# Optimization experiments

Measured on AMD Instinct MI355X. Metric: run time of the kernel, lower is better.

Reference implementation:

```python
import jax, jax.numpy as jnp
import numpy as np

N, E, F, H, C = 50000, 800000, 602, 32, 41
BN_EPS = 1e-5


def _mlp(h, Wa, ba, Wb, bb):
    return jax.nn.relu(h @ Wa + ba) @ Wb + bb


def _bn(h, gamma, beta):
    # BatchNorm1d training mode: per-feature batch mean / biased variance
    m = jnp.mean(h, axis=0)
    v = jnp.var(h, axis=0)
    return (h - m) * jax.lax.rsqrt(v + BN_EPS) * gamma + beta


def _gin(x, row, col, Wa, ba, Wb, bb):
    # sum-aggregate neighbor features (SpMM via gather + segment_sum), eps=0
    agg = jax.ops.segment_sum(x[col], row, num_segments=x.shape[0])
    return _mlp(x + agg, Wa, ba, Wb, bb)


def setup_inputs() -> dict:
    key = jax.random.key(0)
    ks = jax.random.split(key, 16)
    s = 0.05
    inp = {
        "x": jax.random.normal(ks[0], (N, F), dtype=jnp.float32),
        "row": jax.random.randint(ks[1], (E,), 0, N),
        "col": jax.random.randint(ks[2], (E,), 0, N),
        # conv1 MLP
        "W1a": jax.random.normal(ks[3], (F, H), dtype=jnp.float32) * s,
        "b1a": jnp.zeros((H,), jnp.float32),
        "W1b": jax.random.normal(ks[4], (H, H), dtype=jnp.float32) * s,
        "b1b": jnp.zeros((H,), jnp.float32),
        "g1": jnp.ones((H,), jnp.float32),
        "be1": jnp.zeros((H,), jnp.float32),
        # conv2 MLP
        "W2a": jax.random.normal(ks[5], (H, H), dtype=jnp.float32) * s,
        "b2a": jnp.zeros((H,), jnp.float32),
        "W2b": jax.random.normal(ks[6], (H, H), dtype=jnp.float32) * s,
        "b2b": jnp.zeros((H,), jnp.float32),
        "g2": jnp.ones((H,), jnp.float32),
        "be2": jnp.zeros((H,), jnp.float32),
        # heads
        "Wf1": jax.random.normal(ks[7], (H, H), dtype=jnp.float32) * s,
        "bf1": jnp.zeros((H,), jnp.float32),
        "Wf2": jax.random.normal(ks[8], (H, C), dtype=jnp.float32) * s,
        "bf2": jnp.zeros((C,), jnp.float32),
    }
    return inp


def reference(x, row, col, W1a, b1a, W1b, b1b, g1, be1,
              W2a, b2a, W2b, b2b, g2, be2, Wf1, bf1, Wf2, bf2):
    h = _bn(_gin(x, row, col, W1a, b1a, W1b, b1b), g1, be1)
    h = _bn(_gin(h, row, col, W2a, b2a, W2b, b2b), g2, be2)
    h = jax.nn.relu(h @ Wf1 + bf1)
    return h @ Wf2 + bf2
```

## Files before the change

### kernel.cpp

```cpp
#include <hip/hip_runtime.h>
#include <hip/hip_bf16.h>

#define N_NODES 50000
#define F_IN    602
#define H_DIM   32
#define C_OUT   41
#define E_EDGES 800000
#define BN_EPS  1e-5f

__global__ __launch_bounds__(256) void k_gemm_in_v3(
    const float* __restrict__ x, const float* __restrict__ W,
    float* __restrict__ p) {
  __shared__ float xs[64 * 68];
  __shared__ float ws[32 * 68];
  const int tid = threadIdx.x;
  const int r0 = blockIdx.x * 64;

  const int cg  = tid & 15;
  const int rgg = tid >> 4;

  const int srow = tid >> 5;
  const int fe   = tid & 31;

  const float* xrp[8];
  #pragma unroll
  for (int pp = 0; pp < 8; pp++) {
    int rr = r0 + pp * 8 + srow;
    if (rr > N_NODES - 1) rr = N_NODES - 1;
    xrp[pp] = x + (size_t)rr * F_IN;
  }

  float2 xr[8];
  float4 wr[2];

  #pragma unroll
  for (int pp = 0; pp < 8; pp++)
    xr[pp] = *(const float2*)(xrp[pp] + 2 * fe);
  #pragma unroll
  for (int q = 0; q < 2; q++)
    wr[q] = *(const float4*)(W + q * 1024 + 4 * tid);

  float acc[4][2] = {};

  for (int ch = 0; ch < 10; ch++) {
    __syncthreads();
    #pragma unroll
    for (int pp = 0; pp < 8; pp++)
      *(float2*)&xs[(pp * 8 + srow) * 68 + 2 * fe] = xr[pp];
    #pragma unroll
    for (int q = 0; q < 2; q++) {
      int off = q * 1024 + 4 * tid;
      int kk = off >> 5, c0 = off & 31;
      ws[(c0 + 0) * 68 + kk] = wr[q].x;
      ws[(c0 + 1) * 68 + kk] = wr[q].y;
      ws[(c0 + 2) * 68 + kk] = wr[q].z;
      ws[(c0 + 3) * 68 + kk] = wr[q].w;
    }
    __syncthreads();
    if (ch < 9) {
      const int k0 = (ch + 1) * 64;
      #pragma unroll
      for (int pp = 0; pp < 8; pp++) {
        int k = k0 + 2 * fe;
        float2 v = {0.f, 0.f};
        if (k + 2 <= F_IN) v = *(const float2*)(xrp[pp] + k);
        xr[pp] = v;
      }
      #pragma unroll
      for (int q = 0; q < 2; q++) {
        int off = k0 * H_DIM + q * 1024 + 4 * tid;
        float4 v = {0.f, 0.f, 0.f, 0.f};
        if (off < F_IN * H_DIM) v = *(const float4*)(W + off);
        wr[q] = v;
      }
    }
    #pragma unroll
    for (int kq = 0; kq < 16; kq++) {
      float4 xv[4], wv[2];
      #pragma unroll
      for (int i = 0; i < 4; i++) xv[i] = *(float4*)&xs[(rgg + 16 * i) * 68 + kq * 4];
      #pragma unroll
      for (int j = 0; j < 2; j++) wv[j] = *(float4*)&ws[(cg + 16 * j) * 68 + kq * 4];
      #pragma unroll
      for (int i = 0; i < 4; i++)
        #pragma unroll
        for (int j = 0; j < 2; j++)
          acc[i][j] += xv[i].x * wv[j].x + xv[i].y * wv[j].y +
                       xv[i].z * wv[j].z + xv[i].w * wv[j].w;
    }
  }

  #pragma unroll
  for (int i = 0; i < 4; i++) {
    int gr = r0 + rgg + 16 * i;
    if (gr < N_NODES) {
      #pragma unroll
      for (int j = 0; j < 2; j++)
        p[(size_t)gr * H_DIM + cg + 16 * j] = acc[i][j];
    }
  }
}

__global__ __launch_bounds__(256) void k_hist(const int* __restrict__ row,
                                              int* __restrict__ deg) {
  int e = blockIdx.x * 256 + threadIdx.x;
  if (e < E_EDGES) atomicAdd(&deg[row[e]], 1);
}

__global__ __launch_bounds__(256) void k_scanA(const int* __restrict__ deg,
                                               int* __restrict__ start,
                                               int* __restrict__ bsum) {
  __shared__ int sc[256];
  int t = threadIdx.x, i = blockIdx.x * 256 + t;
  int v = (i < N_NODES) ? deg[i] : 0;
  sc[t] = v;
  __syncthreads();
  #pragma unroll
  for (int off = 1; off < 256; off <<= 1) {
    int u = (t >= off) ? sc[t - off] : 0;
    __syncthreads();
    sc[t] += u;
    __syncthreads();
  }
  if (i < N_NODES) start[i] = sc[t] - v;
  if (t == 255) bsum[blockIdx.x] = sc[255];
}

__global__ __launch_bounds__(256) void k_scanB(const int* __restrict__ bsum,
                                               int* __restrict__ boff, int nb) {
  __shared__ int sc[256];
  int t = threadIdx.x;
  int v = (t < nb) ? bsum[t] : 0;
  sc[t] = v;
  __syncthreads();
  #pragma unroll
  for (int off = 1; off < 256; off <<= 1) {
    int u = (t >= off) ? sc[t - off] : 0;
    __syncthreads();
    sc[t] += u;
    __syncthreads();
  }
  if (t < nb) boff[t] = sc[t] - v;
}

__global__ __launch_bounds__(256) void k_scanC(int* __restrict__ start,
                                               const int* __restrict__ boff,
                                               int* __restrict__ cursor) {
  int i = blockIdx.x * 256 + threadIdx.x;
  if (i < N_NODES) {
    int s = start[i] + boff[blockIdx.x];
    start[i] = s;
    cursor[i] = s;
  }
  if (i == 0) start[N_NODES] = E_EDGES;
}

__global__ __launch_bounds__(256) void k_fill(const int* __restrict__ row,
                                              const int* __restrict__ col,
                                              int* __restrict__ cursor,
                                              int* __restrict__ ecol) {
  int e = blockIdx.x * 256 + threadIdx.x;
  if (e < E_EDGES) {
    int pos = atomicAdd(&cursor[row[e]], 1);
    ecol[pos] = col[e];
  }
}

__global__ __launch_bounds__(256) void k_gather(
    const float* __restrict__ p, const float* __restrict__ b,
    const int* __restrict__ start, const int* __restrict__ ecol,
    float* __restrict__ z) {
  int hw = (blockIdx.x * 256 + threadIdx.x) >> 5;
  int c = threadIdx.x & 31;
  if (hw >= N_NODES) return;
  int s = start[hw], e = start[hw + 1];
  float acc = p[(size_t)hw * H_DIM + c] + b[c];
  int i = s;
  for (; i + 3 < e; i += 4) {
    int s0 = ecol[i], s1 = ecol[i + 1], s2 = ecol[i + 2], s3 = ecol[i + 3];
    float v0 = p[(size_t)s0 * H_DIM + c];
    float v1 = p[(size_t)s1 * H_DIM + c];
    float v2 = p[(size_t)s2 * H_DIM + c];
    float v3 = p[(size_t)s3 * H_DIM + c];
    acc += v0; acc += v1; acc += v2; acc += v3;
  }
  for (; i < e; i++) acc += p[(size_t)ecol[i] * H_DIM + c];
  z[(size_t)hw * H_DIM + c] = acc;
}

__global__ __launch_bounds__(256) void k_zinit(const float* __restrict__ p,
                                               const float* __restrict__ b,
                                               float* __restrict__ z) {
  int i = blockIdx.x * 256 + threadIdx.x;
  if (i < N_NODES * H_DIM) z[i] = p[i] + b[i & 31];
}

__global__ __launch_bounds__(256) void k_scatter(
    const int* __restrict__ row, const int* __restrict__ col,
    const float* __restrict__ p, float* __restrict__ z) {
  long long t = (long long)blockIdx.x * 256 + threadIdx.x;
  int e = (int)(t >> 5);
  int c = (int)(t & 31);
  if (e < E_EDGES) {
    int s = col[e], d = row[e];
    atomicAdd(&z[(size_t)d * H_DIM + c], p[(size_t)s * H_DIM + c]);
  }
}

__global__ __launch_bounds__(256) void k_mlp_stats(
    const float* __restrict__ z, const float* __restrict__ W,
    const float* __restrict__ b, float* __restrict__ hpre,
    float* __restrict__ stats) {
  __shared__ float as_[64 * 36];
  __shared__ float ws[32 * 36];
  __shared__ float red[512];
  const int tid = threadIdx.x;
  for (int i = tid; i < 1024; i += 256) {
    int k = i >> 5, c = i & 31;
    ws[c * 36 + k] = W[(size_t)k * H_DIM + c];
  }
  const int r0 = blockIdx.x * 64;
  for (int i = tid; i < 2048; i += 256) {
    int r = i >> 5, c = i & 31;
    int gr = r0 + r;
    float v = (gr < N_NODES) ? z[(size_t)gr * H_DIM + c] : 0.f;
    as_[r * 36 + c] = fmaxf(v, 0.f);
  }
  __syncthreads();
  const int c = tid & 31, rg = tid >> 5;
  float4 wc[8];
  #pragma unroll
  for (int q = 0; q < 8; q++) wc[q] = *(float4*)&ws[c * 36 + q * 4];
  const float bc = b[c];
  float lsum = 0.f, lsq = 0.f;
  #pragma unroll
  for (int i = 0; i < 8; i++) {
    int r = rg * 8 + i;
    float a = bc;
    #pragma unroll
    for (int q = 0; q < 8; q++) {
      float4 h4 = *(float4*)&as_[r * 36 + q * 4];
      a += h4.x * wc[q].x + h4.y * wc[q].y + h4.z * wc[q].z + h4.w * wc[q].w;
    }
    int gr = r0 + r;
    if (gr < N_NODES) {
      hpre[(size_t)gr * H_DIM + c] = a;
      lsum += a; lsq += a * a;
    }
  }
  __syncthreads();
  red[tid] = lsum; red[256 + tid] = lsq;
  __syncthreads();
  if (tid < 32) {
    float s = 0.f, q = 0.f;
    #pragma unroll
    for (int g = 0; g < 8; g++) { s += red[g * 32 + tid]; q += red[256 + g * 32 + tid]; }
    atomicAdd(&stats[tid], s);
    atomicAdd(&stats[32 + tid], q);
  }
}

__global__ __launch_bounds__(256) void k_gemm32_affine(
    const float* __restrict__ hpre, const float* __restrict__ stats,
    const float* __restrict__ g, const float* __restrict__ be,
    const float* __restrict__ W, float* __restrict__ p) {
  __shared__ float hs[64 * 36];
  __shared__ float ws[32 * 36];
  __shared__ float ssl[64];
  const int tid = threadIdx.x;
  if (tid < 32) {
    float m = stats[tid] * (1.f / N_NODES);
    float v = stats[32 + tid] * (1.f / N_NODES) - m * m;
    float sc = g[tid] * rsqrtf(v + BN_EPS);
    ssl[tid] = sc;
    ssl[32 + tid] = be[tid] - m * sc;
  }
  for (int i = tid; i < 1024; i += 256) {
    int k = i >> 5, c = i & 31;
    ws[c * 36 + k] = W[(size_t)k * H_DIM + c];
  }
  __syncthreads();
  const int r0 = blockIdx.x * 64;
  for (int i = tid; i < 2048; i += 256) {
    int r = i >> 5, c = i & 31;
    int gr = r0 + r;
    float v = (gr < N_NODES) ? hpre[(size_t)gr * H_DIM + c] * ssl[c] + ssl[32 + c] : 0.f;
    hs[r * 36 + c] = v;
  }
  __syncthreads();
  const int c = tid & 31, rg = tid >> 5;
  float4 wc[8];
  #pragma unroll
  for (int q = 0; q < 8; q++) wc[q] = *(float4*)&ws[c * 36 + q * 4];
  #pragma unroll
  for (int i = 0; i < 8; i++) {
    int r = rg * 8 + i;
    float a = 0.f;
    #pragma unroll
    for (int q = 0; q < 8; q++) {
      float4 h4 = *(float4*)&hs[r * 36 + q * 4];
      a += h4.x * wc[q].x + h4.y * wc[q].y + h4.z * wc[q].z + h4.w * wc[q].w;
    }
    int gr = r0 + r;
    if (gr < N_NODES) p[(size_t)gr * H_DIM + c] = a;
  }
}

__global__ __launch_bounds__(256) void k_heads(
    const float* __restrict__ hpre, const float* __restrict__ stats,
    const float* __restrict__ g, const float* __restrict__ be,
    const float* __restrict__ W1, const float* __restrict__ b1,
    const float* __restrict__ W2, const float* __restrict__ b2,
    float* __restrict__ out) {
  __shared__ float hs[64 * 36];
  __shared__ float fs[64 * 36];
  __shared__ float w1[32 * 36];
  __shared__ float w2[41 * 36];
  __shared__ float ssl[64];
  const int tid = threadIdx.x;
  if (tid < 32) {
    float m = stats[tid] * (1.f / N_NODES);
    float v = stats[32 + tid] * (1.f / N_NODES) - m * m;
    float sc = g[tid] * rsqrtf(v + BN_EPS);
    ssl[tid] = sc;
    ssl[32 + tid] = be[tid] - m * sc;
  }
  for (int i = tid; i < 1024; i += 256) {
    int k = i >> 5, c = i & 31;
    w1[c * 36 + k] = W1[(size_t)k * H_DIM + c];
  }
  for (int i = tid; i < 41 * 32; i += 256) {
    int j = i >> 5, k = i & 31;
    w2[j * 36 + k] = W2[(size_t)k * C_OUT + j];
  }
  __syncthreads();
  const int r0 = blockIdx.x * 64;
  for (int i = tid; i < 2048; i += 256) {
    int r = i >> 5, c = i & 31;
    int gr = r0 + r;
    hs[r * 36 + c] = (gr < N_NODES) ? hpre[(size_t)gr * H_DIM + c] * ssl[c] + ssl[32 + c] : 0.f;
  }
  __syncthreads();
  {
    const int c = tid & 31, rg = tid >> 5;
    float4 wc[8];
    #pragma unroll
    for (int q = 0; q < 8; q++) wc[q] = *(float4*)&w1[c * 36 + q * 4];
    const float bc = b1[c];
    #pragma unroll
    for (int i = 0; i < 8; i++) {
      int r = rg * 8 + i;
      float a = bc;
      #pragma unroll
      for (int q = 0; q < 8; q++) {
        float4 h4 = *(float4*)&hs[r * 36 + q * 4];
        a += h4.x * wc[q].x + h4.y * wc[q].y + h4.z * wc[q].z + h4.w * wc[q].w;
      }
      fs[r * 36 + c] = fmaxf(a, 0.f);
    }
  }
  __syncthreads();
  for (int idx = tid; idx < 64 * C_OUT; idx += 256) {
    int r = idx / C_OUT, j = idx - r * C_OUT;
    int gr = r0 + r;
    if (gr < N_NODES) {
      float a = b2[j];
      #pragma unroll
      for (int q = 0; q < 8; q++) {
        float4 f4 = *(float4*)&fs[r * 36 + q * 4];
        float4 w4 = *(float4*)&w2[j * 36 + q * 4];
        a += f4.x * w4.x + f4.y * w4.y + f4.z * w4.z + f4.w * w4.w;
      }
      out[(size_t)gr * C_OUT + j] = a;
    }
  }
}

extern "C" void kernel_launch(void* const* d_in, const int* in_sizes, int n_in,
                              void* d_out, int out_size, void* d_ws, size_t ws_size,
                              hipStream_t stream) {
  const float* x   = (const float*)d_in[0];
  const int* row   = (const int*)d_in[1];
  const int* col   = (const int*)d_in[2];
  const float* W1a = (const float*)d_in[3];
  const float* b1a = (const float*)d_in[4];
  const float* W1b = (const float*)d_in[5];
  const float* b1b = (const float*)d_in[6];
  const float* g1  = (const float*)d_in[7];
  const float* be1 = (const float*)d_in[8];
  const float* W2a = (const float*)d_in[9];
  const float* b2a = (const float*)d_in[10];
  const float* W2b = (const float*)d_in[11];
  const float* b2b = (const float*)d_in[12];
  const float* g2  = (const float*)d_in[13];
  const float* be2 = (const float*)d_in[14];
  const float* Wf1 = (const float*)d_in[15];
  const float* bf1 = (const float*)d_in[16];
  const float* Wf2 = (const float*)d_in[17];
  const float* bf2 = (const float*)d_in[18];
  float* out = (float*)d_out;

  float* ws = (float*)d_ws;
  const size_t NH = (size_t)N_NODES * H_DIM;
  float* pA    = ws;
  float* zB    = ws + NH;
  float* hC    = ws + 2 * NH;
  float* stats = ws + 3 * NH;
  int*   startA = (int*)(ws + 3 * NH + 256);
  int*   cursor = startA + 50016;
  int*   deg    = cursor + 50016;
  int*   ecol   = deg + 50016;
  int*   bsum   = ecol + E_EDGES;
  int*   boff   = bsum + 256;
  const size_t need_bytes = ((3 * NH + 256) + 3 * 50016 + E_EDGES + 512) * 4;
  const bool use_csr = (ws_size >= need_bytes);

  hipMemsetAsync(stats, 0, 128 * sizeof(float), stream);

  const int g64   = (N_NODES + 63) / 64;
  const int gE    = (E_EDGES + 255) / 256;
  const int gN    = (N_NODES + 255) / 256;
  const int gHW   = (N_NODES * 32 + 255) / 256;
  const int gScat = (E_EDGES * 32 + 255) / 256;

  if (use_csr) {
    hipMemsetAsync(deg, 0, 50000 * sizeof(int), stream);
    k_hist <<<gE, 256, 0, stream>>>(row, deg);
    k_scanA<<<gN, 256, 0, stream>>>(deg, startA, bsum);
    k_scanB<<<1, 256, 0, stream>>>(bsum, boff, gN);
    k_scanC<<<gN, 256, 0, stream>>>(startA, boff, cursor);
    k_fill <<<gE, 256, 0, stream>>>(row, col, cursor, ecol);
  }

  k_gemm_in_v3<<<g64, 256, 0, stream>>>(x, W1a, pA);
  if (use_csr) {
    k_gather<<<gHW, 256, 0, stream>>>(pA, b1a, startA, ecol, zB);
  } else {
    k_zinit<<<g64 * 8, 256, 0, stream>>>(pA, b1a, zB);
    k_scatter<<<gScat, 256, 0, stream>>>(row, col, pA, zB);
  }
  k_mlp_stats<<<g64, 256, 0, stream>>>(zB, W1b, b1b, hC, stats);
  k_gemm32_affine<<<g64, 256, 0, stream>>>(hC, stats, g1, be1, W2a, pA);
  if (use_csr) {
    k_gather<<<gHW, 256, 0, stream>>>(pA, b2a, startA, ecol, zB);
  } else {
    k_zinit<<<g64 * 8, 256, 0, stream>>>(pA, b2a, zB);
    k_scatter<<<gScat, 256, 0, stream>>>(row, col, pA, zB);
  }
  k_mlp_stats<<<g64, 256, 0, stream>>>(zB, W2b, b2b, hC, stats + 64);
  k_heads<<<g64, 256, 0, stream>>>(hC, stats + 64, g2, be2, Wf1, bf1, Wf2, bf2, out);
}
```

Measured before the change: 483.8 us.

## Use split-bf16 MFMA for input GEMM, fuse weight prep with histogram

Replaces the FP32 LDS-tiled input projection with a matrix-core kernel. Each fp32 value is split into high and low bf16 parts and three MFMA products are summed to keep roughly fp32 accuracy. A new prep kernel pre-transposes and splits W1a, and is fused into the same launch as the degree histogram. The two memsets are merged into one, and the gather loop gains an 8-way unrolled path for more memory-level parallelism. The cost is three times the MFMA work, a slight change in numerics, and direct global loads of x with no LDS staging.

```diff
diff --git a/kernel.cpp b/kernel.cpp
--- a/kernel.cpp
+++ b/kernel.cpp
@@ -7,104 +7,107 @@
 #define C_OUT   41
 #define E_EDGES 800000
 #define BN_EPS  1e-5f
-
-__global__ __launch_bounds__(256) void k_gemm_in_v3(
-    const float* __restrict__ x, const float* __restrict__ W,
-    float* __restrict__ p) {
-  __shared__ float xs[64 * 68];
-  __shared__ float ws[32 * 68];
+#define KPAD    608
+
+typedef short bf16x8 __attribute__((ext_vector_type(8)));
+typedef float f32x4  __attribute__((ext_vector_type(4)));
+
+__device__ inline unsigned short f2bf(float f) {
+  unsigned int u = __builtin_bit_cast(unsigned int, f);
+  unsigned int r = (u + 0x7FFFu + ((u >> 16) & 1u)) >> 16;
+  return (unsigned short)r;
+}
+
+__global__ __launch_bounds__(256) void k_prep(
+    const float* __restrict__ W, unsigned short* __restrict__ wt_hi,
+    unsigned short* __restrict__ wt_lo, const int* __restrict__ row,
+    int* __restrict__ deg) {
+  const int b = blockIdx.x;
+  if (b < 76) {
+    int idx = b * 256 + threadIdx.x;
+    int k = idx >> 5, c = idx & 31;
+    unsigned short h = 0, l = 0;
+    if (k < F_IN) {
+      float v = W[(size_t)k * H_DIM + c];
+      h = f2bf(v);
+      float fh = __builtin_bit_cast(float, (unsigned int)h << 16);
+      l = f2bf(v - fh);
+    }
+    if (k < KPAD) { wt_hi[c * KPAD + k] = h; wt_lo[c * KPAD + k] = l; }
+  } else {
+    int e = (b - 76) * 256 + threadIdx.x;
+    if (e < E_EDGES) atomicAdd(&deg[row[e]], 1);
+  }
+}
+
+__global__ __launch_bounds__(256) void k_gemm_mfma2(
+    const float* __restrict__ x, const unsigned short* __restrict__ wt_hi,
+    const unsigned short* __restrict__ wt_lo, float* __restrict__ p) {
   const int tid = threadIdx.x;
+  const int wv = tid >> 6, ln = tid & 63;
+  const int m = ln & 15, q = ln >> 4;
   const int r0 = blockIdx.x * 64;
-
-  const int cg  = tid & 15;
-  const int rgg = tid >> 4;
-
-  const int srow = tid >> 5;
-  const int fe   = tid & 31;
-
-  const float* xrp[8];
-  #pragma unroll
-  for (int pp = 0; pp < 8; pp++) {
-    int rr = r0 + pp * 8 + srow;
-    if (rr > N_NODES - 1) rr = N_NODES - 1;
-    xrp[pp] = x + (size_t)rr * F_IN;
-  }
-
-  float2 xr[8];
-  float4 wr[2];
-
-  #pragma unroll
-  for (int pp = 0; pp < 8; pp++)
-    xr[pp] = *(const float2*)(xrp[pp] + 2 * fe);
-  #pragma unroll
-  for (int q = 0; q < 2; q++)
-    wr[q] = *(const float4*)(W + q * 1024 + 4 * tid);
-
-  float acc[4][2] = {};
-
-  for (int ch = 0; ch < 10; ch++) {
-    __syncthreads();
-    #pragma unroll
-    for (int pp = 0; pp < 8; pp++)
-      *(float2*)&xs[(pp * 8 + srow) * 68 + 2 * fe] = xr[pp];
-    #pragma unroll
-    for (int q = 0; q < 2; q++) {
-      int off = q * 1024 + 4 * tid;
-      int kk = off >> 5, c0 = off & 31;
-      ws[(c0 + 0) * 68 + kk] = wr[q].x;
-      ws[(c0 + 1) * 68 + kk] = wr[q].y;
-      ws[(c0 + 2) * 68 + kk] = wr[q].z;
-      ws[(c0 + 3) * 68 + kk] = wr[q].w;
-    }
-    __syncthreads();
-    if (ch < 9) {
-      const int k0 = (ch + 1) * 64;
+  int rowl = r0 + 16 * wv + m;
+  if (rowl > N_NODES - 1) rowl = N_NODES - 1;
+  const float* xrow = x + (size_t)rowl * F_IN;
+  const unsigned short* pb0h = wt_hi + m * KPAD;
+  const unsigned short* pb0l = wt_lo + m * KPAD;
+  const unsigned short* pb1h = wt_hi + (m + 16) * KPAD;
+  const unsigned short* pb1l = wt_lo + (m + 16) * KPAD;
+
+  f32x4 acc0 = {0.f, 0.f, 0.f, 0.f};
+  f32x4 acc1 = {0.f, 0.f, 0.f, 0.f};
+
+  float xf[8];
+  auto load_x = [&](int ch) {
+    const int k = ch * 32 + 8 * q;
+    if (ch == 18 && q == 3) {
+      float2 v = *(const float2*)(xrow + 600);
+      xf[0] = v.x; xf[1] = v.y;
+      xf[2] = 0.f; xf[3] = 0.f; xf[4] = 0.f; xf[5] = 0.f; xf[6] = 0.f; xf[7] = 0.f;
+    } else {
       #pragma unroll
-      for (int pp = 0; pp < 8; pp++) {
-        int k = k0 + 2 * fe;
-        float2 v = {0.f, 0.f};
-        if (k + 2 <= F_IN) v = *(const float2*)(xrp[pp] + k);
-        xr[pp] = v;
+      for (int j = 0; j < 4; j++) {
+        float2 v = *(const float2*)(xrow + k + 2 * j);
+        xf[2 * j] = v.x; xf[2 * j + 1] = v.y;
       }
-      #pragma unroll
-      for (int q = 0; q < 2; q++) {
-        int off = k0 * H_DIM + q * 1024 + 4 * tid;
-        float4 v = {0.f, 0.f, 0.f, 0.f};
-        if (off < F_IN * H_DIM) v = *(const float4*)(W + off);
-        wr[q] = v;
-      }
-    }
-    #pragma unroll
-    for (int kq = 0; kq < 16; kq++) {
-      float4 xv[4], wv[2];
-      #pragma unroll
-      for (int i = 0; i < 4; i++) xv[i] = *(float4*)&xs[(rgg + 16 * i) * 68 + kq * 4];
-      #pragma unroll
-      for (int j = 0; j < 2; j++) wv[j] = *(float4*)&ws[(cg + 16 * j) * 68 + kq * 4];
-      #pragma unroll
-      for (int i = 0; i < 4; i++)
-        #pragma unroll
-        for (int j = 0; j < 2; j++)
-          acc[i][j] += xv[i].x * wv[j].x + xv[i].y * wv[j].y +
-                       xv[i].z * wv[j].z + xv[i].w * wv[j].w;
-    }
-  }
-
-  #pragma unroll
-  for (int i = 0; i < 4; i++) {
-    int gr = r0 + rgg + 16 * i;
-    if (gr < N_NODES) {
-      #pragma unroll
-      for (int j = 0; j < 2; j++)
-        p[(size_t)gr * H_DIM + cg + 16 * j] = acc[i][j];
-    }
-  }
-}
-
-__global__ __launch_bounds__(256) void k_hist(const int* __restrict__ row,
-                                              int* __restrict__ deg) {
-  int e = blockIdx.x * 256 + threadIdx.x;
-  if (e < E_EDGES) atomicAdd(&deg[row[e]], 1);
+    }
+  };
+
+  load_x(0);
+
+  for (int ch = 0; ch < 19; ch++) {
+    bf16x8 ah, al;
+    #pragma unroll
+    for (int j = 0; j < 8; j++) {
+      unsigned short h = f2bf(xf[j]);
+      float fh = __builtin_bit_cast(float, (unsigned int)h << 16);
+      unsigned short lo = f2bf(xf[j] - fh);
+      ah[j] = (short)h;
+      al[j] = (short)lo;
+    }
+    if (ch < 18) load_x(ch + 1);
+    const int koff = ch * 32 + 8 * q;
+    bf16x8 b0h = *(const bf16x8*)(pb0h + koff);
+    bf16x8 b0l = *(const bf16x8*)(pb0l + koff);
+    bf16x8 b1h = *(const bf16x8*)(pb1h + koff);
+    bf16x8 b1l = *(const bf16x8*)(pb1l + koff);
+    acc0 = __builtin_amdgcn_mfma_f32_16x16x32_bf16(ah, b0h, acc0, 0, 0, 0);
+    acc1 = __builtin_amdgcn_mfma_f32_16x16x32_bf16(ah, b1h, acc1, 0, 0, 0);
+    acc0 = __builtin_amdgcn_mfma_f32_16x16x32_bf16(al, b0h, acc0, 0, 0, 0);
+    acc1 = __builtin_amdgcn_mfma_f32_16x16x32_bf16(al, b1h, acc1, 0, 0, 0);
+    acc0 = __builtin_amdgcn_mfma_f32_16x16x32_bf16(ah, b0l, acc0, 0, 0, 0);
+    acc1 = __builtin_amdgcn_mfma_f32_16x16x32_bf16(ah, b1l, acc1, 0, 0, 0);
+  }
+
+  #pragma unroll
+  for (int reg = 0; reg < 4; reg++) {
+    int rowg = r0 + 16 * wv + q * 4 + reg;
+    if (rowg < N_NODES) {
+      p[(size_t)rowg * H_DIM + m]      = acc0[reg];
+      p[(size_t)rowg * H_DIM + m + 16] = acc1[reg];
+    }
+  }
 }
 
 __global__ __launch_bounds__(256) void k_scanA(const int* __restrict__ deg,
@@ -176,6 +179,20 @@
   int s = start[hw], e = start[hw + 1];
   float acc = p[(size_t)hw * H_DIM + c] + b[c];
   int i = s;
+  for (; i + 7 < e; i += 8) {
+    int s0 = ecol[i],     s1 = ecol[i + 1], s2 = ecol[i + 2], s3 = ecol[i + 3];
+    int s4 = ecol[i + 4], s5 = ecol[i + 5], s6 = ecol[i + 6], s7 = ecol[i + 7];
+    float v0 = p[(size_t)s0 * H_DIM + c];
+    float v1 = p[(size_t)s1 * H_DIM + c];
+    float v2 = p[(size_t)s2 * H_DIM + c];
+    float v3 = p[(size_t)s3 * H_DIM + c];
+    float v4 = p[(size_t)s4 * H_DIM + c];
+    float v5 = p[(size_t)s5 * H_DIM + c];
+    float v6 = p[(size_t)s6 * H_DIM + c];
+    float v7 = p[(size_t)s7 * H_DIM + c];
+    acc += v0; acc += v1; acc += v2; acc += v3;
+    acc += v4; acc += v5; acc += v6; acc += v7;
+  }
   for (; i + 3 < e; i += 4) {
     int s0 = ecol[i], s1 = ecol[i + 1], s2 = ecol[i + 2], s3 = ecol[i + 3];
     float v0 = p[(size_t)s0 * H_DIM + c];
@@ -406,16 +423,18 @@
   float* zB    = ws + NH;
   float* hC    = ws + 2 * NH;
   float* stats = ws + 3 * NH;
-  int*   startA = (int*)(ws + 3 * NH + 256);
+  int*   deg    = (int*)(stats + 128);
+  int*   startA = deg + 50016;
   int*   cursor = startA + 50016;
-  int*   deg    = cursor + 50016;
-  int*   ecol   = deg + 50016;
+  int*   ecol   = cursor + 50016;
   int*   bsum   = ecol + E_EDGES;
   int*   boff   = bsum + 256;
-  const size_t need_bytes = ((3 * NH + 256) + 3 * 50016 + E_EDGES + 512) * 4;
-  const bool use_csr = (ws_size >= need_bytes);
-
-  hipMemsetAsync(stats, 0, 128 * sizeof(float), stream);
+  const size_t csr_need = ((3 * NH + 128) + 3 * 50016 + E_EDGES + 512) * 4
+                          + 2 * KPAD * 32 * 2;
+  const bool use_csr = (ws_size >= csr_need);
+  unsigned short* wt_hi = use_csr ? (unsigned short*)(boff + 256)
+                                  : (unsigned short*)(stats + 128);
+  unsigned short* wt_lo = wt_hi + KPAD * 32;
 
   const int g64   = (N_NODES + 63) / 64;
   const int gE    = (E_EDGES + 255) / 256;
@@ -424,29 +443,30 @@
   const int gScat = (E_EDGES * 32 + 255) / 256;
 
   if (use_csr) {
-    hipMemsetAsync(deg, 0, 50000 * sizeof(int), stream);
-    k_hist <<<gE, 256, 0, stream>>>(row, deg);
+    hipMemsetAsync(stats, 0, (128 + 50016) * sizeof(int), stream);
+    k_prep <<<76 + gE, 256, 0, stream>>>(W1a, wt_hi, wt_lo, row, deg);
     k_scanA<<<gN, 256, 0, stream>>>(deg, startA, bsum);
     k_scanB<<<1, 256, 0, stream>>>(bsum, boff, gN);
     k_scanC<<<gN, 256, 0, stream>>>(startA, boff, cursor);
     k_fill <<<gE, 256, 0, stream>>>(row, col, cursor, ecol);
-  }
-
-  k_gemm_in_v3<<<g64, 256, 0, stream>>>(x, W1a, pA);
-  if (use_csr) {
+    k_gemm_mfma2<<<g64, 256, 0, stream>>>(x, wt_hi, wt_lo, pA);
     k_gather<<<gHW, 256, 0, stream>>>(pA, b1a, startA, ecol, zB);
+    k_mlp_stats<<<g64, 256, 0, stream>>>(zB, W1b, b1b, hC, stats);
+    k_gemm32_affine<<<g64, 256, 0, stream>>>(hC, stats, g1, be1, W2a, pA);
+    k_gather<<<gHW, 256, 0, stream>>>(pA, b2a, startA, ecol, zB);
+    k_mlp_stats<<<g64, 256, 0, stream>>>(zB, W2b, b2b, hC, stats + 64);
+    k_heads<<<g64, 256, 0, stream>>>(hC, stats + 64, g2, be2, Wf1, bf1, Wf2, bf2, out);
   } else {
+    hipMemsetAsync(stats, 0, 128 * sizeof(float), stream);
+    k_prep <<<76, 256, 0, stream>>>(W1a, wt_hi, wt_lo, row, (int*)nullptr);
+    k_gemm_mfma2<<<g64, 256, 0, stream>>>(x, wt_hi, wt_lo, pA);
     k_zinit<<<g64 * 8, 256, 0, stream>>>(pA, b1a, zB);
     k_scatter<<<gScat, 256, 0, stream>>>(row, col, pA, zB);
-  }
-  k_mlp_stats<<<g64, 256, 0, stream>>>(zB, W1b, b1b, hC, stats);
-  k_gemm32_affine<<<g64, 256, 0, stream>>>(hC, stats, g1, be1, W2a, pA);
-  if (use_csr) {
-    k_gather<<<gHW, 256, 0, stream>>>(pA, b2a, startA, ecol, zB);
-  } else {
+    k_mlp_stats<<<g64, 256, 0, stream>>>(zB, W1b, b1b, hC, stats);
+    k_gemm32_affine<<<g64, 256, 0, stream>>>(hC, stats, g1, be1, W2a, pA);
     k_zinit<<<g64 * 8, 256, 0, stream>>>(pA, b2a, zB);
     k_scatter<<<gScat, 256, 0, stream>>>(row, col, pA, zB);
-  }
-  k_mlp_stats<<<g64, 256, 0, stream>>>(zB, W2b, b2b, hC, stats + 64);
-  k_heads<<<g64, 256, 0, stream>>>(hC, stats + 64, g2, be2, Wf1, bf1, Wf2, bf2, out);
-}
+    k_mlp_stats<<<g64, 256, 0, stream>>>(zB, W2b, b2b, hC, stats + 64);
+    k_heads<<<g64, 256, 0, stream>>>(hC, stats + 64, g2, be2, Wf1, bf1, Wf2, bf2, out);
+  }
+}
```

New measurement: 454.9 us. 1.06x faster.
